# Kernel optimization log

Measured on AMD Instinct MI355X. Metric: run time of the kernel, lower is better.

The kernel has to match this reference:

```python
import jax, jax.numpy as jnp
import numpy as np

DIM = 2048
BATCH = 64


def setup_inputs() -> dict:
    key = jax.random.key(0)
    kx, kq, kk, kv = jax.random.split(key, 4)
    s = 1.0 / np.sqrt(DIM).astype(np.float32)  # keep q*k logits O(1)
    x = jax.random.normal(kx, (BATCH, DIM), dtype=jnp.float32)
    Wq = jax.random.normal(kq, (DIM, DIM), dtype=jnp.float32) * s
    Wk = jax.random.normal(kk, (DIM, DIM), dtype=jnp.float32) * s
    Wv = jax.random.normal(kv, (DIM, DIM), dtype=jnp.float32) * s
    return {"x": x, "Wq": Wq, "Wk": Wk, "Wv": Wv}


def reference(x, Wq, Wk, Wv):
    # nn.Linear(dim, inner_dim, bias=False): y = x @ W.T, W: [inner_dim, dim]
    q = x @ Wq.T  # [b, N]  (head_dim = 1, so each token's q is a scalar)
    k = x @ Wk.T  # [b, N]
    v = x @ Wv.T  # [b, N]
    # dot[b,i,j] = q[b,i] * k[b,j]  (rank-1 outer product per batch)
    logits = q[:, :, None] * k[:, None, :]  # [b, N, N]
    attn = jax.nn.softmax(logits, axis=-1)
    out = jnp.einsum("bij,bj->bi", attn, v)  # [b, N]
    # dim == inner_dim -> scale is Identity
    return out
```

## Files before the change

kernel.cpp:

```cpp
#include <hip/hip_runtime.h>
#include <hip/hip_bf16.h>

#define DIM 2048
#define NB  64
#define KSL 4
#define JSL 4

typedef short bf16x8 __attribute__((ext_vector_type(8)));
typedef short s16x4  __attribute__((ext_vector_type(4)));
typedef float f32x4  __attribute__((ext_vector_type(4)));
typedef float f32x2  __attribute__((ext_vector_type(2)));

__device__ __forceinline__ unsigned short f32_to_bf16_rne(float f) {
  unsigned u = __builtin_bit_cast(unsigned, f);
  unsigned r = u + 0x7FFF + ((u >> 16) & 1);
  return (unsigned short)(r >> 16);
}

__global__ __launch_bounds__(256)
void prep(const float* __restrict__ x, unsigned short* __restrict__ xrh,
          unsigned short* __restrict__ xrl) {
  const int tg = blockIdx.x * 256 + threadIdx.x;
  const int b = tg >> 9;
  const int k = (tg & 511) * 4;
  float4 f = *(const float4*)(x + (size_t)b * DIM + k);
  const int mt = b >> 4, l15 = b & 15;
  const int ck = k >> 5, quad = (k >> 3) & 3, u = k & 7;
  const size_t off = (((size_t)(mt * 64 + ck) * 64) + quad * 16 + l15) * 8 + u;
  float vf[4] = {f.x, f.y, f.z, f.w};
  ushort4 h4, l4;
  unsigned short* hp = &h4.x;
  unsigned short* lp = &l4.x;
#pragma unroll
  for (int e = 0; e < 4; ++e) {
    unsigned short h = f32_to_bf16_rne(vf[e]);
    float hf = __builtin_bit_cast(float, ((unsigned)h) << 16);
    hp[e] = h;
    lp[e] = f32_to_bf16_rne(vf[e] - hf);
  }
  *(ushort4*)(xrh + off) = h4;
  *(ushort4*)(xrl + off) = l4;
}

#define WSTR 260

__device__ __forceinline__ void conv_store_w(short (*wh)[WSTR], short (*wl)[WSTR],
                                             const float4* wreg, int wave, int lane) {
#pragma unroll
  for (int p = 0; p < 8; ++p) {
    const int r = p * 4 + wave;
    float wf[4] = {wreg[p].x, wreg[p].y, wreg[p].z, wreg[p].w};
    s16x4 h4, l4;
#pragma unroll
    for (int e = 0; e < 4; ++e) {
      unsigned uu = __builtin_bit_cast(unsigned, wf[e]);
      h4[e] = (short)(uu >> 16);
      float hf = __builtin_bit_cast(float, uu & 0xFFFF0000u);
      float res = wf[e] - hf;
      l4[e] = (short)(__builtin_bit_cast(unsigned, res) >> 16);
    }
    *(s16x4*)&wh[r][lane * 4] = h4;
    *(s16x4*)&wl[r][lane * 4] = l4;
  }
}

__global__ __launch_bounds__(256)
void qkv_mfma(const unsigned short* __restrict__ xrh,
              const unsigned short* __restrict__ xrl,
              const float* __restrict__ Wq, const float* __restrict__ Wk,
              const float* __restrict__ Wv, float* __restrict__ part) {
  const int mat = blockIdx.z;
  const float* __restrict__ W = (mat == 0) ? Wq : ((mat == 1) ? Wk : Wv);
  const int t = threadIdx.x;
  const int wave = t >> 6, lane = t & 63;
  const int l15 = lane & 15, quad = lane >> 4;
  const int j0 = blockIdx.x * 32;
  const int kb0 = blockIdx.y * 512;

  __shared__ __align__(16) short wh[32][WSTR];
  __shared__ __align__(16) short wl[32][WSTR];

  const int jh = wave & 1;
  const int mh = wave >> 1;
  const int frow = jh * 16 + l15;
  f32x4 acc[2] = {{0.f,0.f,0.f,0.f},{0.f,0.f,0.f,0.f}};

  float4 wa[8], wb[8];
#pragma unroll
  for (int p = 0; p < 8; ++p)
    wa[p] = *(const float4*)(W + (size_t)(j0 + p * 4 + wave) * DIM + kb0 + lane * 4);

#pragma unroll
  for (int c = 0; c < 2; ++c) {
    if (c == 0) conv_store_w(wh, wl, wa, wave, lane);
    else        conv_store_w(wh, wl, wb, wave, lane);
    if (c == 0) {
#pragma unroll
      for (int p = 0; p < 8; ++p)
        wb[p] = *(const float4*)(W + (size_t)(j0 + p * 4 + wave) * DIM +
                                 kb0 + 256 + lane * 4);
    }
    __syncthreads();

    const int ckb = blockIdx.y * 16 + c * 8;
#pragma unroll
    for (int kk = 0; kk < 8; ++kk) {
      bf16x8 whf, wlf;
      *(s16x4*)&whf       = *(const s16x4*)&wh[frow][kk * 32 + quad * 8];
      *(((s16x4*)&whf)+1) = *(const s16x4*)&wh[frow][kk * 32 + quad * 8 + 4];
      *(s16x4*)&wlf       = *(const s16x4*)&wl[frow][kk * 32 + quad * 8];
      *(((s16x4*)&wlf)+1) = *(const s16x4*)&wl[frow][kk * 32 + quad * 8 + 4];
      const int ck = ckb + kk;
#pragma unroll
      for (int u = 0; u < 2; ++u) {
        const int mt = mh * 2 + u;
        const size_t xo = (((size_t)(mt * 64 + ck)) * 64 + lane) * 8;
        bf16x8 ah = *(const bf16x8*)(xrh + xo);
        bf16x8 al = *(const bf16x8*)(xrl + xo);
        acc[u] = __builtin_amdgcn_mfma_f32_16x16x32_bf16(ah, whf, acc[u], 0, 0, 0);
        acc[u] = __builtin_amdgcn_mfma_f32_16x16x32_bf16(al, whf, acc[u], 0, 0, 0);
        acc[u] = __builtin_amdgcn_mfma_f32_16x16x32_bf16(ah, wlf, acc[u], 0, 0, 0);
      }
    }
    if (c == 0) __syncthreads();
  }

  float* __restrict__ pb =
      part + ((size_t)(blockIdx.y * 3 + mat) * NB) * DIM + j0 + jh * 16 + l15;
#pragma unroll
  for (int u = 0; u < 2; ++u)
#pragma unroll
    for (int r = 0; r < 4; ++r) {
      const int b = (mh * 2 + u) * 16 + quad * 4 + r;
      pb[(size_t)b * DIM] = acc[u][r];
    }
}

__global__ __launch_bounds__(256)
void attn(const float* __restrict__ part, f32x2* __restrict__ pnd) {
  const int b = blockIdx.z, js = blockIdx.y, t = threadIdx.x;
  const int i = blockIdx.x * 256 + t;
  const int jb = js * (DIM / JSL), j2 = t * 2;

  __shared__ __align__(16) float ks[DIM / JSL];
  __shared__ __align__(16) float vs[DIM / JSL];

  float kx = 0.f, ky = 0.f, vx = 0.f, vy = 0.f, qi = 0.f;
#pragma unroll
  for (int sl = 0; sl < KSL; ++sl) {
    const float* __restrict__ pk = part + ((size_t)(sl * 3 + 1) * NB + b) * DIM + jb;
    const float* __restrict__ pv = part + ((size_t)(sl * 3 + 2) * NB + b) * DIM + jb;
    float2 a  = *(const float2*)(pk + j2);
    float2 c2 = *(const float2*)(pv + j2);
    kx += a.x; ky += a.y; vx += c2.x; vy += c2.y;
    qi += part[((size_t)(sl * 3 + 0) * NB + b) * DIM + i];
  }
  *(float2*)(ks + j2) = make_float2(kx, ky);
  *(float2*)(vs + j2) = make_float2(vx, vy);
  __syncthreads();

  const float c = qi * 1.4426950408889634f;
  f32x2 num0 = {0.f, 0.f}, num1 = {0.f, 0.f};
  f32x2 den0 = {0.f, 0.f}, den1 = {0.f, 0.f};
#pragma unroll 4
  for (int j = 0; j < DIM / JSL; j += 8) {
    float4 k0 = *(const float4*)(ks + j);
    float4 k1 = *(const float4*)(ks + j + 4);
    float4 v0 = *(const float4*)(vs + j);
    float4 v1 = *(const float4*)(vs + j + 4);
    f32x2 e0, e1, e2, e3;
    e0.x = __builtin_amdgcn_exp2f(c * k0.x);
    e0.y = __builtin_amdgcn_exp2f(c * k0.y);
    e1.x = __builtin_amdgcn_exp2f(c * k0.z);
    e1.y = __builtin_amdgcn_exp2f(c * k0.w);
    e2.x = __builtin_amdgcn_exp2f(c * k1.x);
    e2.y = __builtin_amdgcn_exp2f(c * k1.y);
    e3.x = __builtin_amdgcn_exp2f(c * k1.z);
    e3.y = __builtin_amdgcn_exp2f(c * k1.w);
    den0 += e0; den1 += e1; den0 += e2; den1 += e3;
    f32x2 va = {v0.x, v0.y}, vb = {v0.z, v0.w};
    f32x2 vc = {v1.x, v1.y}, vd = {v1.z, v1.w};
    num0 = __builtin_elementwise_fma(e0, va, num0);
    num1 = __builtin_elementwise_fma(e1, vb, num1);
    num0 = __builtin_elementwise_fma(e2, vc, num0);
    num1 = __builtin_elementwise_fma(e3, vd, num1);
  }
  f32x2 nd;
  nd.x = (num0.x + num0.y) + (num1.x + num1.y);
  nd.y = (den0.x + den0.y) + (den1.x + den1.y);
  pnd[((size_t)b * JSL + js) * DIM + i] = nd;
}

__global__ __launch_bounds__(256)
void attn_fin(const f32x2* __restrict__ pnd, float* __restrict__ out) {
  const int b = blockIdx.y;
  const int i = blockIdx.x * 256 + threadIdx.x;
  float n = 0.f, d = 0.f;
#pragma unroll
  for (int s = 0; s < JSL; ++s) {
    f32x2 p = pnd[((size_t)b * JSL + s) * DIM + i];
    n += p.x; d += p.y;
  }
  out[(size_t)b * DIM + i] = n / d;
}

extern "C" void kernel_launch(void* const* d_in, const int* in_sizes, int n_in,
                              void* d_out, int out_size, void* d_ws, size_t ws_size,
                              hipStream_t stream) {
  const float* x  = (const float*)d_in[0];
  const float* Wq = (const float*)d_in[1];
  const float* Wk = (const float*)d_in[2];
  const float* Wv = (const float*)d_in[3];
  float* out = (float*)d_out;

  char* w = (char*)d_ws;
  unsigned short* xrh = (unsigned short*)w;
  unsigned short* xrl = (unsigned short*)(w + (512 << 10));
  float* part = (float*)(w + (1 << 20));
  f32x2* pnd  = (f32x2*)(w + (16 << 20));

  hipLaunchKernelGGL(prep, dim3(128), dim3(256), 0, stream, x, xrh, xrl);
  hipLaunchKernelGGL(qkv_mfma, dim3(64, KSL, 3), dim3(256), 0, stream,
                     xrh, xrl, Wq, Wk, Wv, part);
  hipLaunchKernelGGL(attn, dim3(8, JSL, NB), dim3(256), 0, stream, part, pnd);
  hipLaunchKernelGGL(attn_fin, dim3(8, NB), dim3(256), 0, stream, pnd, out);
}
```

Before: 133.8 us.

## Reduce split-K partials with atomics and read K/V directly in attention

The QKV GEMM now accumulates its split-K partial results into one zero-initialized qkv buffer with float atomicAdd, instead of writing separate partial slices that the attention kernel summed. The zeroing is folded into the prep kernel. The attention kernel drops its shared-memory staging and sync and reads K/V straight from global memory with wave-uniform (broadcast) loads. The j-split goes from 4 to 2, which halves the partial numerator/denominator traffic but also halves the attention grid. The atomics add contention and make the summation order nondeterministic.

```diff
diff --git a/kernel.cpp b/kernel.cpp
--- a/kernel.cpp
+++ b/kernel.cpp
@@ -4,7 +4,7 @@
 #define DIM 2048
 #define NB  64
 #define KSL 4
-#define JSL 4
+#define JSL 2
 
 typedef short bf16x8 __attribute__((ext_vector_type(8)));
 typedef short s16x4  __attribute__((ext_vector_type(4)));
@@ -19,8 +19,12 @@
 
 __global__ __launch_bounds__(256)
 void prep(const float* __restrict__ x, unsigned short* __restrict__ xrh,
-          unsigned short* __restrict__ xrl) {
+          unsigned short* __restrict__ xrl, float* __restrict__ qkv) {
   const int tg = blockIdx.x * 256 + threadIdx.x;
+#pragma unroll
+  for (int z = 0; z < 3; ++z)
+    *(float4*)(qkv + ((size_t)z * 32768 + tg) * 4) = make_float4(0.f,0.f,0.f,0.f);
+
   const int b = tg >> 9;
   const int k = (tg & 511) * 4;
   float4 f = *(const float4*)(x + (size_t)b * DIM + k);
@@ -68,7 +72,7 @@
 void qkv_mfma(const unsigned short* __restrict__ xrh,
               const unsigned short* __restrict__ xrl,
               const float* __restrict__ Wq, const float* __restrict__ Wk,
-              const float* __restrict__ Wv, float* __restrict__ part) {
+              const float* __restrict__ Wv, float* __restrict__ qkv) {
   const int mat = blockIdx.z;
   const float* __restrict__ W = (mat == 0) ? Wq : ((mat == 1) ? Wk : Wv);
   const int t = threadIdx.x;
@@ -125,69 +129,42 @@
     if (c == 0) __syncthreads();
   }
 
-  float* __restrict__ pb =
-      part + ((size_t)(blockIdx.y * 3 + mat) * NB) * DIM + j0 + jh * 16 + l15;
+  float* __restrict__ pb = qkv + (size_t)mat * NB * DIM + j0 + jh * 16 + l15;
 #pragma unroll
   for (int u = 0; u < 2; ++u)
 #pragma unroll
     for (int r = 0; r < 4; ++r) {
       const int b = (mh * 2 + u) * 16 + quad * 4 + r;
-      pb[(size_t)b * DIM] = acc[u][r];
-    }
-}
-
-__global__ __launch_bounds__(256)
-void attn(const float* __restrict__ part, f32x2* __restrict__ pnd) {
-  const int b = blockIdx.z, js = blockIdx.y, t = threadIdx.x;
-  const int i = blockIdx.x * 256 + t;
-  const int jb = js * (DIM / JSL), j2 = t * 2;
-
-  __shared__ __align__(16) float ks[DIM / JSL];
-  __shared__ __align__(16) float vs[DIM / JSL];
-
-  float kx = 0.f, ky = 0.f, vx = 0.f, vy = 0.f, qi = 0.f;
-#pragma unroll
-  for (int sl = 0; sl < KSL; ++sl) {
-    const float* __restrict__ pk = part + ((size_t)(sl * 3 + 1) * NB + b) * DIM + jb;
-    const float* __restrict__ pv = part + ((size_t)(sl * 3 + 2) * NB + b) * DIM + jb;
-    float2 a  = *(const float2*)(pk + j2);
-    float2 c2 = *(const float2*)(pv + j2);
-    kx += a.x; ky += a.y; vx += c2.x; vy += c2.y;
-    qi += part[((size_t)(sl * 3 + 0) * NB + b) * DIM + i];
-  }
-  *(float2*)(ks + j2) = make_float2(kx, ky);
-  *(float2*)(vs + j2) = make_float2(vx, vy);
-  __syncthreads();
-
+      atomicAdd(pb + (size_t)b * DIM, acc[u][r]);
+    }
+}
+
+__global__ __launch_bounds__(256)
+void attn(const float* __restrict__ qkv, f32x2* __restrict__ pnd) {
+  const int b = blockIdx.z, js = blockIdx.y;
+  const int i = blockIdx.x * 256 + threadIdx.x;
+  const float qi = qkv[(size_t)b * DIM + i];
   const float c = qi * 1.4426950408889634f;
-  f32x2 num0 = {0.f, 0.f}, num1 = {0.f, 0.f};
-  f32x2 den0 = {0.f, 0.f}, den1 = {0.f, 0.f};
-#pragma unroll 4
+  const float* __restrict__ kp = qkv + (size_t)(NB + b) * DIM + js * (DIM / JSL);
+  const float* __restrict__ vp = qkv + (size_t)(2 * NB + b) * DIM + js * (DIM / JSL);
+
+  float num[4] = {0.f, 0.f, 0.f, 0.f};
+  float den[4] = {0.f, 0.f, 0.f, 0.f};
+#pragma unroll 2
   for (int j = 0; j < DIM / JSL; j += 8) {
-    float4 k0 = *(const float4*)(ks + j);
-    float4 k1 = *(const float4*)(ks + j + 4);
-    float4 v0 = *(const float4*)(vs + j);
-    float4 v1 = *(const float4*)(vs + j + 4);
-    f32x2 e0, e1, e2, e3;
-    e0.x = __builtin_amdgcn_exp2f(c * k0.x);
-    e0.y = __builtin_amdgcn_exp2f(c * k0.y);
-    e1.x = __builtin_amdgcn_exp2f(c * k0.z);
-    e1.y = __builtin_amdgcn_exp2f(c * k0.w);
-    e2.x = __builtin_amdgcn_exp2f(c * k1.x);
-    e2.y = __builtin_amdgcn_exp2f(c * k1.y);
-    e3.x = __builtin_amdgcn_exp2f(c * k1.z);
-    e3.y = __builtin_amdgcn_exp2f(c * k1.w);
-    den0 += e0; den1 += e1; den0 += e2; den1 += e3;
-    f32x2 va = {v0.x, v0.y}, vb = {v0.z, v0.w};
-    f32x2 vc = {v1.x, v1.y}, vd = {v1.z, v1.w};
-    num0 = __builtin_elementwise_fma(e0, va, num0);
-    num1 = __builtin_elementwise_fma(e1, vb, num1);
-    num0 = __builtin_elementwise_fma(e2, vc, num0);
-    num1 = __builtin_elementwise_fma(e3, vd, num1);
+    float kb[8], vb[8];
+#pragma unroll
+    for (int u = 0; u < 8; ++u) { kb[u] = kp[j + u]; vb[u] = vp[j + u]; }
+#pragma unroll
+    for (int u = 0; u < 8; ++u) {
+      float e = __builtin_amdgcn_exp2f(c * kb[u]);
+      den[u & 3] += e;
+      num[u & 3] = fmaf(e, vb[u], num[u & 3]);
+    }
   }
   f32x2 nd;
-  nd.x = (num0.x + num0.y) + (num1.x + num1.y);
-  nd.y = (den0.x + den0.y) + (den1.x + den1.y);
+  nd.x = (num[0] + num[1]) + (num[2] + num[3]);
+  nd.y = (den[0] + den[1]) + (den[2] + den[3]);
   pnd[((size_t)b * JSL + js) * DIM + i] = nd;
 }
 
@@ -216,12 +193,12 @@
   char* w = (char*)d_ws;
   unsigned short* xrh = (unsigned short*)w;
   unsigned short* xrl = (unsigned short*)(w + (512 << 10));
-  float* part = (float*)(w + (1 << 20));
-  f32x2* pnd  = (f32x2*)(w + (16 << 20));
-
-  hipLaunchKernelGGL(prep, dim3(128), dim3(256), 0, stream, x, xrh, xrl);
+  float* qkv = (float*)(w + (1 << 20));
+  f32x2* pnd = (f32x2*)(w + (4 << 20));
+
+  hipLaunchKernelGGL(prep, dim3(128), dim3(256), 0, stream, x, xrh, xrl, qkv);
   hipLaunchKernelGGL(qkv_mfma, dim3(64, KSL, 3), dim3(256), 0, stream,
-                     xrh, xrl, Wq, Wk, Wv, part);
-  hipLaunchKernelGGL(attn, dim3(8, JSL, NB), dim3(256), 0, stream, part, pnd);
+                     xrh, xrl, Wq, Wk, Wv, qkv);
+  hipLaunchKernelGGL(attn, dim3(8, JSL, NB), dim3(256), 0, stream, qkv, pnd);
   hipLaunchKernelGGL(attn_fin, dim3(8, NB), dim3(256), 0, stream, pnd, out);
 }
```

Result: slower. 145.1 us (+8.5%).
